# Performance work log

Hardware: AMD Instinct MI355X
Metric: run time of the kernel (lower is better)

Reference implementation:

```python
import jax, jax.numpy as jnp
import numpy as np

N_ATOMS = 8_000_000
N_REC = 2_000_000
N_POC = 500_000
N_CHAINS = 4


def setup_inputs() -> dict:
    key = jax.random.key(0)
    k1, k2, k3, k4 = jax.random.split(key, 4)
    # coordinates in nm, inside a ~5 nm box
    positions = jax.random.uniform(k1, (N_ATOMS, 3), dtype=jnp.float32) * 5.0
    box_vectors = jnp.diag(jnp.array([5.0, 5.0, 5.0], dtype=jnp.float32))
    # unique receptor atom indices into positions
    rec_indices = jax.random.permutation(k2, N_ATOMS)[:N_REC].astype(jnp.int32)
    # unique pocket indices INTO THE REC ARRAY (poc_pos = rec_pos[poc_indices])
    poc_indices = jax.random.permutation(k3, N_REC)[:N_POC].astype(jnp.int32)
    # contiguous chain assignment over rec atoms, all chains present in pocket
    chain_ids = ((jnp.arange(N_REC, dtype=jnp.int32) * N_CHAINS) // N_REC).astype(jnp.int32)
    poc_chain_ids = chain_ids[poc_indices]
    ref_poc = jax.random.uniform(k4, (N_POC, 3), dtype=jnp.float32) * 5.0
    k = jnp.float32(100.0)  # kJ/mol/nm^2
    return {
        "positions": positions, "box_vectors": box_vectors, "ref_poc": ref_poc,
        "k": k, "rec_indices": rec_indices, "poc_indices": poc_indices,
        "chain_ids": chain_ids, "poc_chain_ids": poc_chain_ids, "n_chains": N_CHAINS,
    }


def best_periodic_translation(pos1, pos2, box_vectors):
    # pos1, pos2: [C,3]; box_vectors: [3,3] (rows are lattice vectors)
    delta = pos2 - pos1
    inv = 1.0 / jnp.diag(box_vectors)
    s3 = jnp.round(delta[:, 2] * inv[2])
    delta = delta - s3[:, None] * box_vectors[2]
    s2 = jnp.round(delta[:, 1] * inv[1])
    delta = delta - s2[:, None] * box_vectors[1]
    s1 = jnp.round(delta[:, 0] * inv[0])
    return s1[:, None] * box_vectors[0] + s2[:, None] * box_vectors[1] + s3[:, None] * box_vectors[2]


def reference(positions, box_vectors, ref_poc, k, rec_indices, poc_indices, chain_ids, poc_chain_ids, n_chains):
    rec_pos = positions[rec_indices]  # [R,3]
    # Per-chain pocket COM. NOTE: original indexes global positions here
    # (positions[poc_chain_indices]), NOT rec_pos -- reproduced faithfully.
    poc_glob = positions[poc_indices]  # [P,3]
    counts = jax.ops.segment_sum(jnp.ones((poc_glob.shape[0],), poc_glob.dtype), poc_chain_ids, num_segments=n_chains)  # [C]
    poc_com = jax.ops.segment_sum(poc_glob, poc_chain_ids, num_segments=n_chains) / counts[:, None]  # [C,3]
    ref_com = jax.ops.segment_sum(ref_poc, poc_chain_ids, num_segments=n_chains) / counts[:, None]  # [C,3]
    best_t = best_periodic_translation(poc_com, ref_com, box_vectors)  # [C,3]
    rec_pos = rec_pos + best_t[chain_ids]  # translate each chain into the reference image

    poc_pos = rec_pos[poc_indices]  # [P,3]
    rec_origin = jnp.mean(rec_pos, axis=0)
    rec_centered = rec_pos - rec_origin
    r_sq = jnp.sum(rec_centered ** 2, axis=1)  # [R]
    F = jnp.zeros_like(rec_pos).at[poc_indices].set(-2.0 * k * (poc_pos - ref_poc))
    F_mean = jnp.mean(F, axis=0)
    torque = jnp.cross(rec_centered, F)
    torque_mean = jnp.mean(torque, axis=0)
    F_rot = jnp.cross(torque_mean[None], rec_centered) / r_sq[:, None]
    F_final = jnp.zeros_like(positions).at[rec_indices].set(F_mean + F_rot)
    return (jnp.float32(0.0), F_final)
```

## Files before the change

### kernel.cpp

```cpp
#include <hip/hip_runtime.h>


typedef unsigned int uint32;
typedef unsigned char uchar;

#define MAXC 16
#define W_BT 0
#define W_O 48
#define W_FM 52
#define W_TM 56
#define W_ACC 64

#define GCOUNT_OFF 4096
#define REC_OFF 8192
#define NB 512
#define BSH 14
#define BUCKET_ATOMS (1 << BSH)
#define CAP 5120
#define INV8_OFF (REC_OFF + NB * CAP * 4)

#define PB 512
#define RB 512
#define K1_KPT 16
#define K1_CHUNK (256 * K1_KPT)

struct PartSh { uint32 hist[NB]; uint32 curs[NB]; uint32 base[NB]; };
struct PocSh  { float red[4][43]; float accL[3 + MAXC * 10]; };
union ShU { PartSh part; PocSh poc; };

__device__ inline float waveSum(float v) {
#pragma unroll
  for (int off = 32; off > 0; off >>= 1) v += __shfl_down(v, off, 64);
  return v;
}

__global__ __launch_bounds__(256) void k_fused(
    const float* __restrict__ pos, const float* __restrict__ ref_poc,
    const int* __restrict__ rec_idx, const int* __restrict__ cid,
    const int* __restrict__ poc_idx, const int* __restrict__ poc_cid,
    const int* __restrict__ ncp, int R, int P,
    uint32* __restrict__ gcount, uint32* __restrict__ grecords,
    float* __restrict__ ws) {
  const int tid = threadIdx.x;
  const int bid = blockIdx.x;
  __shared__ ShU sh;
  const int C = ncp[0];

  if (bid < PB) {
    const int gsz = PB * 256;
    if (C <= 4) {
      float vals[43];
#pragma unroll
      for (int v = 0; v < 43; ++v) vals[v] = 0.f;
      for (int rb = bid * 256 + tid; rb < P; rb += 4 * gsz) {
        int rr[4], i2[4], c2[4], ri[4];
        float g[4][3], p[4][3], rf[4][3];
#pragma unroll
        for (int q = 0; q < 4; ++q) {
          int r = rb + q * gsz;
          rr[q] = (r < P) ? r : -1;
        }
#pragma unroll
        for (int q = 0; q < 4; ++q) {
          int r = (rr[q] < 0) ? 0 : rr[q];
          i2[q] = poc_idx[r];
          c2[q] = poc_cid[r];
        }
#pragma unroll
        for (int q = 0; q < 4; ++q) {
          ri[q] = rec_idx[i2[q]];
          g[q][0] = pos[3 * i2[q] + 0];
          g[q][1] = pos[3 * i2[q] + 1];
          g[q][2] = pos[3 * i2[q] + 2];
        }
#pragma unroll
        for (int q = 0; q < 4; ++q) {
          int r = (rr[q] < 0) ? 0 : rr[q];
          p[q][0] = pos[3 * ri[q] + 0];
          p[q][1] = pos[3 * ri[q] + 1];
          p[q][2] = pos[3 * ri[q] + 2];
          rf[q][0] = ref_poc[3 * r + 0];
          rf[q][1] = ref_poc[3 * r + 1];
          rf[q][2] = ref_poc[3 * r + 2];
        }
#pragma unroll
        for (int q = 0; q < 4; ++q) {
          if (rr[q] >= 0) {
            vals[0] += p[q][1] * rf[q][2] - p[q][2] * rf[q][1];
            vals[1] += p[q][2] * rf[q][0] - p[q][0] * rf[q][2];
            vals[2] += p[q][0] * rf[q][1] - p[q][1] * rf[q][0];
#pragma unroll
            for (int cc = 0; cc < 4; ++cc) {
              bool m = (c2[q] == cc);
              float* a = &vals[3 + cc * 10];
              a[0] += m ? g[q][0] : 0.f; a[1] += m ? g[q][1] : 0.f;
              a[2] += m ? g[q][2] : 0.f;
              a[3] += m ? rf[q][0] : 0.f; a[4] += m ? rf[q][1] : 0.f;
              a[5] += m ? rf[q][2] : 0.f;
              a[6] += m ? p[q][0] : 0.f; a[7] += m ? p[q][1] : 0.f;
              a[8] += m ? p[q][2] : 0.f;
              a[9] += m ? 1.f : 0.f;
            }
          }
        }
      }
      const int wid = tid >> 6;
#pragma unroll
      for (int v = 0; v < 43; ++v) {
        float s = waveSum(vals[v]);
        if ((tid & 63) == 0) sh.poc.red[wid][v] = s;
      }
      __syncthreads();
      for (int t = tid; t < 43; t += 256)
        atomicAdd(&ws[W_ACC + 19 + t], sh.poc.red[0][t] + sh.poc.red[1][t] +
                                       sh.poc.red[2][t] + sh.poc.red[3][t]);
    } else {
      float* accL = sh.poc.accL;
      for (int t = tid; t < 3 + MAXC * 10; t += 256) accL[t] = 0.f;
      __syncthreads();
      for (int r = bid * 256 + tid; r < P; r += PB * 256) {
        int i2 = poc_idx[r];
        int c2 = poc_cid[r];
        int ri = rec_idx[i2];
        float gx = pos[3 * i2 + 0], gy = pos[3 * i2 + 1], gz = pos[3 * i2 + 2];
        float px = pos[3 * ri + 0], py = pos[3 * ri + 1], pz = pos[3 * ri + 2];
        float rx = ref_poc[3 * r + 0], ry = ref_poc[3 * r + 1], rz = ref_poc[3 * r + 2];
        atomicAdd(&accL[0], py * rz - pz * ry);
        atomicAdd(&accL[1], pz * rx - px * rz);
        atomicAdd(&accL[2], px * ry - py * rx);
        float* a = &accL[3 + c2 * 10];
        atomicAdd(&a[0], gx); atomicAdd(&a[1], gy); atomicAdd(&a[2], gz);
        atomicAdd(&a[3], rx); atomicAdd(&a[4], ry); atomicAdd(&a[5], rz);
        atomicAdd(&a[6], px); atomicAdd(&a[7], py); atomicAdd(&a[8], pz);
        atomicAdd(&a[9], 1.f);
      }
      __syncthreads();
      for (int t = tid; t < 3 + MAXC * 10; t += 256)
        if (accL[t] != 0.f) atomicAdd(&ws[W_ACC + 19 + t], accL[t]);
    }
  } else {
    const int pb = bid - PB;
    uint32* hist = sh.part.hist;
    uint32* curs = sh.part.curs;
    uint32* base = sh.part.base;
    for (int r0 = pb * K1_CHUNK; r0 < R; r0 += RB * K1_CHUNK) {
      int cnt = R - r0; if (cnt > K1_CHUNK) cnt = K1_CHUNK;
      for (int t = tid; t < NB; t += 256) { hist[t] = 0u; curs[t] = 0u; }
      __syncthreads();
      uint32 enc[K1_KPT];
#pragma unroll
      for (int j = 0; j < K1_KPT; ++j) {
        int t = tid + j * 256;
        uint32 e = 0xFFFFFFFFu;
        if (t < cnt) {
          uint32 idx = (uint32)rec_idx[r0 + t];
          uint32 c = (uint32)cid[r0 + t] & 255u;
          e = (idx << 8) | c;
          atomicAdd(&hist[idx >> BSH], 1u);
        }
        enc[j] = e;
      }
      __syncthreads();
      for (int t = tid; t < NB; t += 256) {
        uint32 h = hist[t];
        base[t] = h ? atomicAdd(&gcount[t], h) : 0u;
      }
      __syncthreads();
#pragma unroll
      for (int j = 0; j < K1_KPT; ++j) {
        uint32 e = enc[j];
        if (e != 0xFFFFFFFFu) {
          uint32 b = e >> (8 + BSH);
          uint32 slot = base[b] + atomicAdd(&curs[b], 1u);
          if (slot < CAP) grecords[b * CAP + slot] = e;
        }
      }
      __syncthreads();
    }
  }
}

__global__ __launch_bounds__(256) void k_bucket_build(
    const float4* __restrict__ pos4, const int* __restrict__ ncp,
    const uint32* __restrict__ gcount, const uint32* __restrict__ grecords,
    int N, uchar* __restrict__ inv8, float* __restrict__ ws) {
  const int tid = threadIdx.x;
  const int b = blockIdx.x;
  const int a0 = b << BSH;
  if (a0 >= N) return;
  int natoms = N - a0; if (natoms > BUCKET_ATOMS) natoms = BUCKET_ATOMS;

  __shared__ uchar map_[BUCKET_ATOMS];
  __shared__ float cnt16[MAXC];
  uint4* m16 = (uint4*)map_;
  uint4 ff; ff.x = ff.y = ff.z = ff.w = 0xFFFFFFFFu;
  for (int t = tid; t < BUCKET_ATOMS / 16; t += 256) m16[t] = ff;
  const int C = ncp[0];
  if (C > 4) for (int t = tid; t < MAXC; t += 256) cnt16[t] = 0.f;
  __syncthreads();

  int n = (int)gcount[b]; if (n > CAP) n = CAP;
  float c0 = 0.f, c1 = 0.f, c2 = 0.f, c3 = 0.f;
  for (int t = tid; t < n; t += 256) {
    uint32 e = grecords[b * CAP + t];
    uint32 ia = (e >> 8) & (BUCKET_ATOMS - 1);
    uint32 c = e & 255u;
    map_[ia] = (uchar)c;
    if (C <= 4) {
      c0 += (c == 0u) ? 1.f : 0.f;
      c1 += (c == 1u) ? 1.f : 0.f;
      c2 += (c == 2u) ? 1.f : 0.f;
      c3 += (c == 3u) ? 1.f : 0.f;
    } else {
      atomicAdd(&cnt16[c], 1.f);
    }
  }
  __syncthreads();

  uchar* dst = inv8 + a0;
  if (natoms == BUCKET_ATOMS) {
    uint4* d16 = (uint4*)dst;
    for (int t = tid; t < BUCKET_ATOMS / 16; t += 256) d16[t] = m16[t];
  } else {
    for (int t = tid; t < natoms; t += 256) dst[t] = map_[t];
  }

  float sx = 0.f, sy = 0.f, sz = 0.f;
  int ngf = natoms >> 2;
  const uchar4* m4 = (const uchar4*)map_;
  int g0 = a0 >> 2;
  for (int g = tid; g < ngf; g += 256) {
    float4 p0 = pos4[3 * (g0 + g) + 0];
    float4 p1 = pos4[3 * (g0 + g) + 1];
    float4 p2 = pos4[3 * (g0 + g) + 2];
    uchar4 m = m4[g];
    if (m.x != 255) { sx += p0.x; sy += p0.y; sz += p0.z; }
    if (m.y != 255) { sx += p0.w; sy += p1.x; sz += p1.y; }
    if (m.z != 255) { sx += p1.z; sy += p1.w; sz += p2.x; }
    if (m.w != 255) { sx += p2.y; sy += p2.z; sz += p2.w; }
  }
  int tb = natoms & 3;
  if (tid < tb) {
    int a = a0 + (ngf << 2) + tid;
    const float* pf = (const float*)pos4;
    if (map_[(ngf << 2) + tid] != 255) {
      sx += pf[3 * a]; sy += pf[3 * a + 1]; sz += pf[3 * a + 2];
    }
  }

  __shared__ float red[4][7];
  float vv[7] = {sx, sy, sz, c0, c1, c2, c3};
  const int wid = tid >> 6;
#pragma unroll
  for (int v = 0; v < 7; ++v) {
    float s = waveSum(vv[v]);
    if ((tid & 63) == 0) red[wid][v] = s;
  }
  __syncthreads();
  if (tid < 7) {
    float s = red[0][tid] + red[1][tid] + red[2][tid] + red[3][tid];
    atomicAdd(&ws[W_ACC + tid], s);
  }
  if (C > 4 && tid < C) atomicAdd(&ws[W_ACC + 3 + tid], cnt16[tid]);
}

__global__ void k_finalize(const float* __restrict__ box,
                           const float* __restrict__ kp,
                           const int* __restrict__ ncp,
                           int R, float* __restrict__ ws) {
  __shared__ float tot[192];
  const int C = ncp[0];
  for (int t = threadIdx.x; t < 192; t += blockDim.x) tot[t] = ws[W_ACC + t];
  __syncthreads();
  if (threadIdx.x != 0) return;
  const float kk = kp[0];
  const float Rf = (float)R;
  const float* xp = &tot[19];
  float inv0 = 1.f / box[0], inv1 = 1.f / box[4], inv2 = 1.f / box[8];
  float ox = tot[0], oy = tot[1], oz = tot[2];
  float Fx = 0, Fy = 0, Fz = 0;
  float T1x = 0, T1y = 0, T1z = 0, T2x = 0, T2y = 0, T2z = 0;
  for (int c = 0; c < C; ++c) {
    float nrec = tot[3 + c];
    const float* a = &tot[22 + c * 10];
    float np = a[9];
    float invn = 1.f / np;
    float pcx = a[0] * invn, pcy = a[1] * invn, pcz = a[2] * invn;
    float rcx = a[3] * invn, rcy = a[4] * invn, rcz = a[5] * invn;
    float dx = rcx - pcx, dy = rcy - pcy, dz = rcz - pcz;
    float s3 = rintf(dz * inv2);
    dx -= s3 * box[6]; dy -= s3 * box[7]; dz -= s3 * box[8];
    float s2 = rintf(dy * inv1);
    dx -= s2 * box[3]; dy -= s2 * box[4]; dz -= s2 * box[5];
    float s1 = rintf(dx * inv0);
    float btx = s1 * box[0] + s2 * box[3] + s3 * box[6];
    float bty = s1 * box[1] + s2 * box[4] + s3 * box[7];
    float btz = s1 * box[2] + s2 * box[5] + s3 * box[8];
    ws[W_BT + c * 3 + 0] = btx;
    ws[W_BT + c * 3 + 1] = bty;
    ws[W_BT + c * 3 + 2] = btz;
    ox += nrec * btx; oy += nrec * bty; oz += nrec * btz;
    float SFx = -2.f * kk * (a[6] + np * btx - a[3]);
    float SFy = -2.f * kk * (a[7] + np * bty - a[4]);
    float SFz = -2.f * kk * (a[8] + np * btz - a[5]);
    Fx += SFx; Fy += SFy; Fz += SFz;
    T1x += a[7] * btz - a[8] * bty;
    T1y += a[8] * btx - a[6] * btz;
    T1z += a[6] * bty - a[7] * btx;
    T2x += bty * SFz - btz * SFy;
    T2y += btz * SFx - btx * SFz;
    T2z += btx * SFy - bty * SFx;
  }
  ox /= Rf; oy /= Rf; oz /= Rf;
  float Tx = 2.f * kk * xp[0] - 2.f * kk * T1x + T2x - (oy * Fz - oz * Fy);
  float Ty = 2.f * kk * xp[1] - 2.f * kk * T1y + T2y - (oz * Fx - ox * Fz);
  float Tz = 2.f * kk * xp[2] - 2.f * kk * T1z + T2z - (ox * Fy - oy * Fx);
  ws[W_O + 0] = ox; ws[W_O + 1] = oy; ws[W_O + 2] = oz;
  ws[W_FM + 0] = Fx / Rf; ws[W_FM + 1] = Fy / Rf; ws[W_FM + 2] = Fz / Rf;
  ws[W_TM + 0] = Tx / Rf; ws[W_TM + 1] = Ty / Rf; ws[W_TM + 2] = Tz / Rf;
}

__global__ __launch_bounds__(256) void k_final_dense(
    const float* __restrict__ pos, const uchar* __restrict__ inv8,
    int N, const float* __restrict__ ws, float* __restrict__ out) {
  __shared__ float stage[3328];
  __shared__ float sc[64];
  const int tid = threadIdx.x;
  if (tid < 64) sc[tid] = ws[tid];
  const int t0 = blockIdx.x * 1024;
  int nat = N - t0; if (nat > 1024) nat = 1024;
  const int nfl = nat * 3;

  if (nat == 1024) {
    const float4* src4 = (const float4*)(pos + 3 * t0);
#pragma unroll
    for (int kk = 0; kk < 3; ++kk) {
      int v4 = tid + kk * 256;
      float4 p = src4[v4];
      int idx = 4 * v4 + v4 / 3;
      stage[idx + 0] = p.x; stage[idx + 1] = p.y;
      stage[idx + 2] = p.z; stage[idx + 3] = p.w;
    }
  } else {
    for (int k = tid; k < nfl; k += 256)
      stage[k + (int)((unsigned)k / 12u)] = pos[3 * t0 + k];
  }
  __syncthreads();

  float ox = sc[W_O + 0], oy = sc[W_O + 1], oz = sc[W_O + 2];
  float fmx = sc[W_FM + 0], fmy = sc[W_FM + 1], fmz = sc[W_FM + 2];
  float tmx = sc[W_TM + 0], tmy = sc[W_TM + 1], tmz = sc[W_TM + 2];

  uchar mc[4];
  if (nat == 1024) {
    uchar4 m = ((const uchar4*)(inv8 + t0))[tid];
    mc[0] = m.x; mc[1] = m.y; mc[2] = m.z; mc[3] = m.w;
  } else {
#pragma unroll
    for (int q = 0; q < 4; ++q) {
      int la = 4 * tid + q;
      mc[q] = (la < nat) ? inv8[t0 + la] : (uchar)255;
    }
  }
#pragma unroll
  for (int q = 0; q < 4; ++q) {
    int la = 4 * tid + q;
    if (la < nat) {
      float* s = &stage[13 * tid + 3 * q];
      float fx = 0.f, fy = 0.f, fz = 0.f;
      int c = mc[q];
      if (c != 255) {
        float cx = s[0] + sc[W_BT + 3 * c + 0] - ox;
        float cy = s[1] + sc[W_BT + 3 * c + 1] - oy;
        float cz = s[2] + sc[W_BT + 3 * c + 2] - oz;
        float inv = 1.f / (cx * cx + cy * cy + cz * cz);
        fx = fmx + (tmy * cz - tmz * cy) * inv;
        fy = fmy + (tmz * cx - tmx * cz) * inv;
        fz = fmz + (tmx * cy - tmy * cx) * inv;
      }
      s[0] = fx; s[1] = fy; s[2] = fz;
    }
  }
  __syncthreads();

  if (blockIdx.x == 0 && tid == 0) out[0] = 0.f;
  float* ob = out + 1 + 3 * t0;
  if (nat == 1024) {
#pragma unroll
    for (int kk = 0; kk < 3; ++kk) {
      int j = tid + kk * 256;
      if (j < 767) {
        int k = 3 + 4 * j;
        float4 v;
        v.x = stage[k + k / 12];
        v.y = stage[(k + 1) + (k + 1) / 12];
        v.z = stage[(k + 2) + (k + 2) / 12];
        v.w = stage[(k + 3) + (k + 3) / 12];
        *(float4*)(ob + k) = v;
      }
    }
    if (tid < 3) ob[tid] = stage[tid];
    if (tid == 3) ob[3071] = stage[3071 + 3071 / 12];
  } else {
    for (int k = tid; k < nfl; k += 256)
      ob[k] = stage[k + (int)((unsigned)k / 12u)];
  }
}

extern "C" void kernel_launch(void* const* d_in, const int* in_sizes, int n_in,
                              void* d_out, int out_size, void* d_ws, size_t ws_size,
                              hipStream_t stream) {
  const float* pos     = (const float*)d_in[0];
  const float* box     = (const float*)d_in[1];
  const float* ref_poc = (const float*)d_in[2];
  const float* kp      = (const float*)d_in[3];
  const int* rec_idx   = (const int*)d_in[4];
  const int* poc_idx   = (const int*)d_in[5];
  const int* cid       = (const int*)d_in[6];
  const int* poc_cid   = (const int*)d_in[7];
  const int* ncp       = (const int*)d_in[8];
  float* out = (float*)d_out;
  float* ws  = (float*)d_ws;
  uint32* gcount   = (uint32*)((char*)d_ws + GCOUNT_OFF);
  uint32* grecords = (uint32*)((char*)d_ws + REC_OFF);
  uchar* inv8      = (uchar*)d_ws + INV8_OFF;

  const int N = in_sizes[0] / 3;
  const int R = in_sizes[4];
  const int P = in_sizes[5];

  hipMemsetAsync(d_ws, 0, 8192, stream);

  k_fused<<<PB + RB, 256, 0, stream>>>(pos, ref_poc, rec_idx, cid, poc_idx,
                                       poc_cid, ncp, R, P, gcount, grecords, ws);
  k_bucket_build<<<NB, 256, 0, stream>>>((const float4*)pos, ncp, gcount,
                                         grecords, N, inv8, ws);
  k_finalize<<<1, 256, 0, stream>>>(box, kp, ncp, R, ws);
  int gF = (N + 1023) / 1024;
  k_final_dense<<<gF, 256, 0, stream>>>(pos, inv8, N, ws, out);
}
```

Before: 267.4 us.

## Restructure kernel pipeline: separate partition, fuse pocket gather with bucket build, fold finalize

The pocket-sum work moves out of the partition kernel and now runs alongside bucket building in one interleaved kernel (even blocks do pocket reduction, odd blocks build buckets). Partition becomes its own kernel sized to the number of chunks. The single-thread finalize kernel is folded into every block of the dense output kernel, which recomputes the scalars redundantly. This removes one launch and the serial one-block stage, and overlaps the two gather-heavy phases. The cost is redundant per-block finalize work and a serialized thread-0 section inside every output block.

```diff
diff --git a/kernel.cpp b/kernel.cpp
--- a/kernel.cpp
+++ b/kernel.cpp
@@ -20,13 +20,12 @@
 #define INV8_OFF (REC_OFF + NB * CAP * 4)
 
 #define PB 512
-#define RB 512
 #define K1_KPT 16
 #define K1_CHUNK (256 * K1_KPT)
 
-struct PartSh { uint32 hist[NB]; uint32 curs[NB]; uint32 base[NB]; };
-struct PocSh  { float red[4][43]; float accL[3 + MAXC * 10]; };
-union ShU { PartSh part; PocSh poc; };
+struct PocSh  { float accL[3 + MAXC * 10]; };
+struct MapSh  { uchar map_[BUCKET_ATOMS]; };
+union ShU { PocSh poc; MapSh map; };
 
 __device__ inline float waveSum(float v) {
 #pragma unroll
@@ -34,25 +33,69 @@
   return v;
 }
 
-__global__ __launch_bounds__(256) void k_fused(
+__global__ __launch_bounds__(256) void k_partition(
+    const int* __restrict__ rec_idx, const int* __restrict__ cid,
+    int R, uint32* __restrict__ gcount, uint32* __restrict__ grecords) {
+  __shared__ uint32 hist[NB];
+  __shared__ uint32 curs[NB];
+  __shared__ uint32 base[NB];
+  const int tid = threadIdx.x;
+  const int r0 = blockIdx.x * K1_CHUNK;
+  int cnt = R - r0; if (cnt > K1_CHUNK) cnt = K1_CHUNK;
+  for (int t = tid; t < NB; t += 256) { hist[t] = 0u; curs[t] = 0u; }
+  __syncthreads();
+  uint32 enc[K1_KPT];
+#pragma unroll
+  for (int j = 0; j < K1_KPT; ++j) {
+    int t = tid + j * 256;
+    uint32 e = 0xFFFFFFFFu;
+    if (t < cnt) {
+      uint32 idx = (uint32)rec_idx[r0 + t];
+      uint32 c = (uint32)cid[r0 + t] & 255u;
+      e = (idx << 8) | c;
+      atomicAdd(&hist[idx >> BSH], 1u);
+    }
+    enc[j] = e;
+  }
+  __syncthreads();
+  for (int t = tid; t < NB; t += 256) {
+    uint32 h = hist[t];
+    base[t] = h ? atomicAdd(&gcount[t], h) : 0u;
+  }
+  __syncthreads();
+#pragma unroll
+  for (int j = 0; j < K1_KPT; ++j) {
+    uint32 e = enc[j];
+    if (e != 0xFFFFFFFFu) {
+      uint32 b = e >> (8 + BSH);
+      uint32 slot = base[b] + atomicAdd(&curs[b], 1u);
+      if (slot < CAP) grecords[b * CAP + slot] = e;
+    }
+  }
+}
+
+__global__ __launch_bounds__(256) void k_gather(
     const float* __restrict__ pos, const float* __restrict__ ref_poc,
-    const int* __restrict__ rec_idx, const int* __restrict__ cid,
+    const int* __restrict__ rec_idx,
     const int* __restrict__ poc_idx, const int* __restrict__ poc_cid,
-    const int* __restrict__ ncp, int R, int P,
-    uint32* __restrict__ gcount, uint32* __restrict__ grecords,
-    float* __restrict__ ws) {
+    const int* __restrict__ ncp, int P, int N,
+    const uint32* __restrict__ gcount, const uint32* __restrict__ grecords,
+    uchar* __restrict__ inv8, float* __restrict__ ws) {
   const int tid = threadIdx.x;
   const int bid = blockIdx.x;
+  const int C = ncp[0];
   __shared__ ShU sh;
-  const int C = ncp[0];
-
-  if (bid < PB) {
+  __shared__ float red[4][43];
+  __shared__ float cnt16[MAXC];
+
+  if ((bid & 1) == 0) {
+    const int pt = bid >> 1;
     const int gsz = PB * 256;
     if (C <= 4) {
       float vals[43];
 #pragma unroll
       for (int v = 0; v < 43; ++v) vals[v] = 0.f;
-      for (int rb = bid * 256 + tid; rb < P; rb += 4 * gsz) {
+      for (int rb = pt * 256 + tid; rb < P; rb += 4 * gsz) {
         int rr[4], i2[4], c2[4], ri[4];
         float g[4][3], p[4][3], rf[4][3];
 #pragma unroll
@@ -108,17 +151,17 @@
 #pragma unroll
       for (int v = 0; v < 43; ++v) {
         float s = waveSum(vals[v]);
-        if ((tid & 63) == 0) sh.poc.red[wid][v] = s;
+        if ((tid & 63) == 0) red[wid][v] = s;
       }
       __syncthreads();
       for (int t = tid; t < 43; t += 256)
-        atomicAdd(&ws[W_ACC + 19 + t], sh.poc.red[0][t] + sh.poc.red[1][t] +
-                                       sh.poc.red[2][t] + sh.poc.red[3][t]);
+        atomicAdd(&ws[W_ACC + 19 + t],
+                  red[0][t] + red[1][t] + red[2][t] + red[3][t]);
     } else {
       float* accL = sh.poc.accL;
       for (int t = tid; t < 3 + MAXC * 10; t += 256) accL[t] = 0.f;
       __syncthreads();
-      for (int r = bid * 256 + tid; r < P; r += PB * 256) {
+      for (int r = pt * 256 + tid; r < P; r += PB * 256) {
         int i2 = poc_idx[r];
         int c2 = poc_cid[r];
         int ri = rec_idx[i2];
@@ -139,197 +182,92 @@
         if (accL[t] != 0.f) atomicAdd(&ws[W_ACC + 19 + t], accL[t]);
     }
   } else {
-    const int pb = bid - PB;
-    uint32* hist = sh.part.hist;
-    uint32* curs = sh.part.curs;
-    uint32* base = sh.part.base;
-    for (int r0 = pb * K1_CHUNK; r0 < R; r0 += RB * K1_CHUNK) {
-      int cnt = R - r0; if (cnt > K1_CHUNK) cnt = K1_CHUNK;
-      for (int t = tid; t < NB; t += 256) { hist[t] = 0u; curs[t] = 0u; }
-      __syncthreads();
-      uint32 enc[K1_KPT];
-#pragma unroll
-      for (int j = 0; j < K1_KPT; ++j) {
-        int t = tid + j * 256;
-        uint32 e = 0xFFFFFFFFu;
-        if (t < cnt) {
-          uint32 idx = (uint32)rec_idx[r0 + t];
-          uint32 c = (uint32)cid[r0 + t] & 255u;
-          e = (idx << 8) | c;
-          atomicAdd(&hist[idx >> BSH], 1u);
-        }
-        enc[j] = e;
-      }
-      __syncthreads();
-      for (int t = tid; t < NB; t += 256) {
-        uint32 h = hist[t];
-        base[t] = h ? atomicAdd(&gcount[t], h) : 0u;
-      }
-      __syncthreads();
-#pragma unroll
-      for (int j = 0; j < K1_KPT; ++j) {
-        uint32 e = enc[j];
-        if (e != 0xFFFFFFFFu) {
-          uint32 b = e >> (8 + BSH);
-          uint32 slot = base[b] + atomicAdd(&curs[b], 1u);
-          if (slot < CAP) grecords[b * CAP + slot] = e;
-        }
-      }
-      __syncthreads();
-    }
+    const int b = bid >> 1;
+    const int a0 = b << BSH;
+    if (a0 >= N) return;
+    int natoms = N - a0; if (natoms > BUCKET_ATOMS) natoms = BUCKET_ATOMS;
+    uchar* map_ = sh.map.map_;
+    uint4* m16 = (uint4*)map_;
+    uint4 ff; ff.x = ff.y = ff.z = ff.w = 0xFFFFFFFFu;
+    for (int t = tid; t < BUCKET_ATOMS / 16; t += 256) m16[t] = ff;
+    if (C > 4) for (int t = tid; t < MAXC; t += 256) cnt16[t] = 0.f;
+    __syncthreads();
+    int n = (int)gcount[b]; if (n > CAP) n = CAP;
+    float c0 = 0.f, c1 = 0.f, c2 = 0.f, c3 = 0.f;
+    for (int t = tid; t < n; t += 256) {
+      uint32 e = grecords[b * CAP + t];
+      uint32 ia = (e >> 8) & (BUCKET_ATOMS - 1);
+      uint32 c = e & 255u;
+      map_[ia] = (uchar)c;
+      if (C <= 4) {
+        c0 += (c == 0u) ? 1.f : 0.f;
+        c1 += (c == 1u) ? 1.f : 0.f;
+        c2 += (c == 2u) ? 1.f : 0.f;
+        c3 += (c == 3u) ? 1.f : 0.f;
+      } else {
+        atomicAdd(&cnt16[c], 1.f);
+      }
+    }
+    __syncthreads();
+    uchar* dst = inv8 + a0;
+    if (natoms == BUCKET_ATOMS) {
+      uint4* d16 = (uint4*)dst;
+      for (int t = tid; t < BUCKET_ATOMS / 16; t += 256) d16[t] = m16[t];
+    } else {
+      for (int t = tid; t < natoms; t += 256) dst[t] = map_[t];
+    }
+    float sx = 0.f, sy = 0.f, sz = 0.f;
+    int ngf = natoms >> 2;
+    const uchar4* m4 = (const uchar4*)map_;
+    const float4* pos4 = (const float4*)pos;
+    int g0 = a0 >> 2;
+    for (int g = tid; g < ngf; g += 256) {
+      float4 p0 = pos4[3 * (g0 + g) + 0];
+      float4 p1 = pos4[3 * (g0 + g) + 1];
+      float4 p2 = pos4[3 * (g0 + g) + 2];
+      uchar4 m = m4[g];
+      if (m.x != 255) { sx += p0.x; sy += p0.y; sz += p0.z; }
+      if (m.y != 255) { sx += p0.w; sy += p1.x; sz += p1.y; }
+      if (m.z != 255) { sx += p1.z; sy += p1.w; sz += p2.x; }
+      if (m.w != 255) { sx += p2.y; sy += p2.z; sz += p2.w; }
+    }
+    int tb = natoms & 3;
+    if (tid < tb) {
+      int a = a0 + (ngf << 2) + tid;
+      if (map_[(ngf << 2) + tid] != 255) {
+        sx += pos[3 * a]; sy += pos[3 * a + 1]; sz += pos[3 * a + 2];
+      }
+    }
+    float vv[7] = {sx, sy, sz, c0, c1, c2, c3};
+    const int wid = tid >> 6;
+#pragma unroll
+    for (int v = 0; v < 7; ++v) {
+      float s = waveSum(vv[v]);
+      if ((tid & 63) == 0) red[wid][v] = s;
+    }
+    __syncthreads();
+    if (tid < 7) {
+      float s = red[0][tid] + red[1][tid] + red[2][tid] + red[3][tid];
+      atomicAdd(&ws[W_ACC + tid], s);
+    }
+    if (C > 4 && tid < C) atomicAdd(&ws[W_ACC + 3 + tid], cnt16[tid]);
   }
 }
 
-__global__ __launch_bounds__(256) void k_bucket_build(
-    const float4* __restrict__ pos4, const int* __restrict__ ncp,
-    const uint32* __restrict__ gcount, const uint32* __restrict__ grecords,
-    int N, uchar* __restrict__ inv8, float* __restrict__ ws) {
-  const int tid = threadIdx.x;
-  const int b = blockIdx.x;
-  const int a0 = b << BSH;
-  if (a0 >= N) return;
-  int natoms = N - a0; if (natoms > BUCKET_ATOMS) natoms = BUCKET_ATOMS;
-
-  __shared__ uchar map_[BUCKET_ATOMS];
-  __shared__ float cnt16[MAXC];
-  uint4* m16 = (uint4*)map_;
-  uint4 ff; ff.x = ff.y = ff.z = ff.w = 0xFFFFFFFFu;
-  for (int t = tid; t < BUCKET_ATOMS / 16; t += 256) m16[t] = ff;
-  const int C = ncp[0];
-  if (C > 4) for (int t = tid; t < MAXC; t += 256) cnt16[t] = 0.f;
-  __syncthreads();
-
-  int n = (int)gcount[b]; if (n > CAP) n = CAP;
-  float c0 = 0.f, c1 = 0.f, c2 = 0.f, c3 = 0.f;
-  for (int t = tid; t < n; t += 256) {
-    uint32 e = grecords[b * CAP + t];
-    uint32 ia = (e >> 8) & (BUCKET_ATOMS - 1);
-    uint32 c = e & 255u;
-    map_[ia] = (uchar)c;
-    if (C <= 4) {
-      c0 += (c == 0u) ? 1.f : 0.f;
-      c1 += (c == 1u) ? 1.f : 0.f;
-      c2 += (c == 2u) ? 1.f : 0.f;
-      c3 += (c == 3u) ? 1.f : 0.f;
-    } else {
-      atomicAdd(&cnt16[c], 1.f);
-    }
-  }
-  __syncthreads();
-
-  uchar* dst = inv8 + a0;
-  if (natoms == BUCKET_ATOMS) {
-    uint4* d16 = (uint4*)dst;
-    for (int t = tid; t < BUCKET_ATOMS / 16; t += 256) d16[t] = m16[t];
-  } else {
-    for (int t = tid; t < natoms; t += 256) dst[t] = map_[t];
-  }
-
-  float sx = 0.f, sy = 0.f, sz = 0.f;
-  int ngf = natoms >> 2;
-  const uchar4* m4 = (const uchar4*)map_;
-  int g0 = a0 >> 2;
-  for (int g = tid; g < ngf; g += 256) {
-    float4 p0 = pos4[3 * (g0 + g) + 0];
-    float4 p1 = pos4[3 * (g0 + g) + 1];
-    float4 p2 = pos4[3 * (g0 + g) + 2];
-    uchar4 m = m4[g];
-    if (m.x != 255) { sx += p0.x; sy += p0.y; sz += p0.z; }
-    if (m.y != 255) { sx += p0.w; sy += p1.x; sz += p1.y; }
-    if (m.z != 255) { sx += p1.z; sy += p1.w; sz += p2.x; }
-    if (m.w != 255) { sx += p2.y; sy += p2.z; sz += p2.w; }
-  }
-  int tb = natoms & 3;
-  if (tid < tb) {
-    int a = a0 + (ngf << 2) + tid;
-    const float* pf = (const float*)pos4;
-    if (map_[(ngf << 2) + tid] != 255) {
-      sx += pf[3 * a]; sy += pf[3 * a + 1]; sz += pf[3 * a + 2];
-    }
-  }
-
-  __shared__ float red[4][7];
-  float vv[7] = {sx, sy, sz, c0, c1, c2, c3};
-  const int wid = tid >> 6;
-#pragma unroll
-  for (int v = 0; v < 7; ++v) {
-    float s = waveSum(vv[v]);
-    if ((tid & 63) == 0) red[wid][v] = s;
-  }
-  __syncthreads();
-  if (tid < 7) {
-    float s = red[0][tid] + red[1][tid] + red[2][tid] + red[3][tid];
-    atomicAdd(&ws[W_ACC + tid], s);
-  }
-  if (C > 4 && tid < C) atomicAdd(&ws[W_ACC + 3 + tid], cnt16[tid]);
-}
-
-__global__ void k_finalize(const float* __restrict__ box,
-                           const float* __restrict__ kp,
-                           const int* __restrict__ ncp,
-                           int R, float* __restrict__ ws) {
+__global__ __launch_bounds__(256) void k_finout(
+    const float* __restrict__ pos, const uchar* __restrict__ inv8,
+    const float* __restrict__ box, const float* __restrict__ kp,
+    const int* __restrict__ ncp, int R, int N,
+    const float* __restrict__ ws, float* __restrict__ out) {
+  __shared__ float stage[3328];
   __shared__ float tot[192];
-  const int C = ncp[0];
-  for (int t = threadIdx.x; t < 192; t += blockDim.x) tot[t] = ws[W_ACC + t];
-  __syncthreads();
-  if (threadIdx.x != 0) return;
-  const float kk = kp[0];
-  const float Rf = (float)R;
-  const float* xp = &tot[19];
-  float inv0 = 1.f / box[0], inv1 = 1.f / box[4], inv2 = 1.f / box[8];
-  float ox = tot[0], oy = tot[1], oz = tot[2];
-  float Fx = 0, Fy = 0, Fz = 0;
-  float T1x = 0, T1y = 0, T1z = 0, T2x = 0, T2y = 0, T2z = 0;
-  for (int c = 0; c < C; ++c) {
-    float nrec = tot[3 + c];
-    const float* a = &tot[22 + c * 10];
-    float np = a[9];
-    float invn = 1.f / np;
-    float pcx = a[0] * invn, pcy = a[1] * invn, pcz = a[2] * invn;
-    float rcx = a[3] * invn, rcy = a[4] * invn, rcz = a[5] * invn;
-    float dx = rcx - pcx, dy = rcy - pcy, dz = rcz - pcz;
-    float s3 = rintf(dz * inv2);
-    dx -= s3 * box[6]; dy -= s3 * box[7]; dz -= s3 * box[8];
-    float s2 = rintf(dy * inv1);
-    dx -= s2 * box[3]; dy -= s2 * box[4]; dz -= s2 * box[5];
-    float s1 = rintf(dx * inv0);
-    float btx = s1 * box[0] + s2 * box[3] + s3 * box[6];
-    float bty = s1 * box[1] + s2 * box[4] + s3 * box[7];
-    float btz = s1 * box[2] + s2 * box[5] + s3 * box[8];
-    ws[W_BT + c * 3 + 0] = btx;
-    ws[W_BT + c * 3 + 1] = bty;
-    ws[W_BT + c * 3 + 2] = btz;
-    ox += nrec * btx; oy += nrec * bty; oz += nrec * btz;
-    float SFx = -2.f * kk * (a[6] + np * btx - a[3]);
-    float SFy = -2.f * kk * (a[7] + np * bty - a[4]);
-    float SFz = -2.f * kk * (a[8] + np * btz - a[5]);
-    Fx += SFx; Fy += SFy; Fz += SFz;
-    T1x += a[7] * btz - a[8] * bty;
-    T1y += a[8] * btx - a[6] * btz;
-    T1z += a[6] * bty - a[7] * btx;
-    T2x += bty * SFz - btz * SFy;
-    T2y += btz * SFx - btx * SFz;
-    T2z += btx * SFy - bty * SFx;
-  }
-  ox /= Rf; oy /= Rf; oz /= Rf;
-  float Tx = 2.f * kk * xp[0] - 2.f * kk * T1x + T2x - (oy * Fz - oz * Fy);
-  float Ty = 2.f * kk * xp[1] - 2.f * kk * T1y + T2y - (oz * Fx - ox * Fz);
-  float Tz = 2.f * kk * xp[2] - 2.f * kk * T1z + T2z - (ox * Fy - oy * Fx);
-  ws[W_O + 0] = ox; ws[W_O + 1] = oy; ws[W_O + 2] = oz;
-  ws[W_FM + 0] = Fx / Rf; ws[W_FM + 1] = Fy / Rf; ws[W_FM + 2] = Fz / Rf;
-  ws[W_TM + 0] = Tx / Rf; ws[W_TM + 1] = Ty / Rf; ws[W_TM + 2] = Tz / Rf;
-}
-
-__global__ __launch_bounds__(256) void k_final_dense(
-    const float* __restrict__ pos, const uchar* __restrict__ inv8,
-    int N, const float* __restrict__ ws, float* __restrict__ out) {
-  __shared__ float stage[3328];
   __shared__ float sc[64];
   const int tid = threadIdx.x;
-  if (tid < 64) sc[tid] = ws[tid];
   const int t0 = blockIdx.x * 1024;
   int nat = N - t0; if (nat > 1024) nat = 1024;
   const int nfl = nat * 3;
+
+  for (int t = tid; t < 192; t += 256) tot[t] = ws[W_ACC + t];
 
   if (nat == 1024) {
     const float4* src4 = (const float4*)(pos + 3 * t0);
@@ -347,9 +285,59 @@
   }
   __syncthreads();
 
-  float ox = sc[W_O + 0], oy = sc[W_O + 1], oz = sc[W_O + 2];
-  float fmx = sc[W_FM + 0], fmy = sc[W_FM + 1], fmz = sc[W_FM + 2];
-  float tmx = sc[W_TM + 0], tmy = sc[W_TM + 1], tmz = sc[W_TM + 2];
+  if (tid == 0) {
+    const int C = ncp[0];
+    const float kk = kp[0];
+    const float Rf = (float)R;
+    const float* xp = &tot[19];
+    float inv0 = 1.f / box[0], inv1 = 1.f / box[4], inv2 = 1.f / box[8];
+    float ox = tot[0], oy = tot[1], oz = tot[2];
+    float Fx = 0, Fy = 0, Fz = 0;
+    float T1x = 0, T1y = 0, T1z = 0, T2x = 0, T2y = 0, T2z = 0;
+    for (int c = 0; c < C; ++c) {
+      float nrec = tot[3 + c];
+      const float* a = &tot[22 + c * 10];
+      float np = a[9];
+      float invn = 1.f / np;
+      float pcx = a[0] * invn, pcy = a[1] * invn, pcz = a[2] * invn;
+      float rcx = a[3] * invn, rcy = a[4] * invn, rcz = a[5] * invn;
+      float dx = rcx - pcx, dy = rcy - pcy, dz = rcz - pcz;
+      float s3 = rintf(dz * inv2);
+      dx -= s3 * box[6]; dy -= s3 * box[7]; dz -= s3 * box[8];
+      float s2 = rintf(dy * inv1);
+      dx -= s2 * box[3]; dy -= s2 * box[4]; dz -= s2 * box[5];
+      float s1 = rintf(dx * inv0);
+      float btx = s1 * box[0] + s2 * box[3] + s3 * box[6];
+      float bty = s1 * box[1] + s2 * box[4] + s3 * box[7];
+      float btz = s1 * box[2] + s2 * box[5] + s3 * box[8];
+      sc[W_BT + c * 3 + 0] = btx;
+      sc[W_BT + c * 3 + 1] = bty;
+      sc[W_BT + c * 3 + 2] = btz;
+      ox += nrec * btx; oy += nrec * bty; oz += nrec * btz;
+      float SFx = -2.f * kk * (a[6] + np * btx - a[3]);
+      float SFy = -2.f * kk * (a[7] + np * bty - a[4]);
+      float SFz = -2.f * kk * (a[8] + np * btz - a[5]);
+      Fx += SFx; Fy += SFy; Fz += SFz;
+      T1x += a[7] * btz - a[8] * bty;
+      T1y += a[8] * btx - a[6] * btz;
+      T1z += a[6] * bty - a[7] * btx;
+      T2x += bty * SFz - btz * SFy;
+      T2y += btz * SFx - btx * SFz;
+      T2z += btx * SFy - bty * SFx;
+    }
+    ox /= Rf; oy /= Rf; oz /= Rf;
+    float Tx = 2.f * kk * xp[0] - 2.f * kk * T1x + T2x - (oy * Fz - oz * Fy);
+    float Ty = 2.f * kk * xp[1] - 2.f * kk * T1y + T2y - (oz * Fx - ox * Fz);
+    float Tz = 2.f * kk * xp[2] - 2.f * kk * T1z + T2z - (ox * Fy - oy * Fx);
+    sc[W_O + 0] = ox; sc[W_O + 1] = oy; sc[W_O + 2] = oz;
+    sc[W_FM + 0] = Fx / Rf; sc[W_FM + 1] = Fy / Rf; sc[W_FM + 2] = Fz / Rf;
+    sc[W_TM + 0] = Tx / Rf; sc[W_TM + 1] = Ty / Rf; sc[W_TM + 2] = Tz / Rf;
+  }
+  __syncthreads();
+
+  const float ox = sc[W_O + 0], oy = sc[W_O + 1], oz = sc[W_O + 2];
+  const float fmx = sc[W_FM + 0], fmy = sc[W_FM + 1], fmz = sc[W_FM + 2];
+  const float tmx = sc[W_TM + 0], tmy = sc[W_TM + 1], tmz = sc[W_TM + 2];
 
   uchar mc[4];
   if (nat == 1024) {
@@ -423,7 +411,7 @@
   float* ws  = (float*)d_ws;
   uint32* gcount   = (uint32*)((char*)d_ws + GCOUNT_OFF);
   uint32* grecords = (uint32*)((char*)d_ws + REC_OFF);
-  uchar* inv8      = (uchar*)d_ws + INV8_OFF;
+  uchar*  inv8     = (uchar*)d_ws + INV8_OFF;
 
   const int N = in_sizes[0] / 3;
   const int R = in_sizes[4];
@@ -431,11 +419,10 @@
 
   hipMemsetAsync(d_ws, 0, 8192, stream);
 
-  k_fused<<<PB + RB, 256, 0, stream>>>(pos, ref_poc, rec_idx, cid, poc_idx,
-                                       poc_cid, ncp, R, P, gcount, grecords, ws);
-  k_bucket_build<<<NB, 256, 0, stream>>>((const float4*)pos, ncp, gcount,
-                                         grecords, N, inv8, ws);
-  k_finalize<<<1, 256, 0, stream>>>(box, kp, ncp, R, ws);
+  const int nchunk = (R + K1_CHUNK - 1) / K1_CHUNK;
+  k_partition<<<nchunk, 256, 0, stream>>>(rec_idx, cid, R, gcount, grecords);
+  k_gather<<<1024, 256, 0, stream>>>(pos, ref_poc, rec_idx, poc_idx, poc_cid,
+                                     ncp, P, N, gcount, grecords, inv8, ws);
   int gF = (N + 1023) / 1024;
-  k_final_dense<<<gF, 256, 0, stream>>>(pos, inv8, N, ws, out);
+  k_finout<<<gF, 256, 0, stream>>>(pos, inv8, box, kp, ncp, R, N, ws, out);
 }
```

New measurement: 270.2 us. Within noise of the previous version (+1.1%).
